# Optimization experiments

Measured on AMD Instinct MI355X. Metric: run time of the kernel, lower is better.

The kernel has to match this reference:

```python
import jax, jax.numpy as jnp
import numpy as np

NH = 16

def sinusoidal_pos(pos, nh=NH):
    # pos: [B, L] -> P: [B, L, nh], interleaved sin/cos with integer multiples of pi
    freqs = jnp.arange(1, nh // 2 + 1, dtype=pos.dtype) * jnp.pi  # [nh/2]
    ang = pos[..., None] * freqs                                   # [B, L, nh/2]
    # interleave: even channels sin, odd channels cos
    P = jnp.stack([jnp.sin(ang), jnp.cos(ang)], axis=-1)           # [B, L, nh/2, 2]
    return P.reshape(*pos.shape, nh)


def setup_inputs() -> dict:
    key = jax.random.key(0)
    k1, k2, k3, k4, k5, k6 = jax.random.split(key, 6)
    B, L, nx, nh = 2048, 1024, 8, NH
    return {
        "x": jax.random.normal(k1, (B, L, nx), dtype=jnp.float32),
        "pos": jax.random.uniform(k2, (B, L), dtype=jnp.float32),
        "W_q": jax.random.normal(k3, (nh, nx), dtype=jnp.float32) * 0.1,
        "W_k": jax.random.normal(k4, (nh, nx), dtype=jnp.float32) * 0.1,
        "W_v": jax.random.normal(k5, (nh, nx), dtype=jnp.float32) * 0.1,
        "W_o": jax.random.normal(k6, (nh, nh), dtype=jnp.float32) * 0.1,
    }


def reference(x, pos, W_q, W_k, W_v, W_o):
    # x: [B, L, nx]; pos: [B, L]; Linear weights are [out, in] (torch convention)
    q = jnp.einsum("blx,hx->blh", x, W_q)
    k = jnp.einsum("blx,hx->blh", x, W_k)
    v = jnp.einsum("blx,hx->blh", x, W_v)
    P = sinusoidal_pos(pos, W_q.shape[0])
    q = q + P
    k = k + P
    L = q.shape[1]
    # channel-wise attention: score over feature dim, [B, nh, nh]
    score = jnp.einsum("bld,ble->bde", q, k) / jnp.sqrt(jnp.asarray(L, q.dtype))
    attn = jax.nn.softmax(score, axis=-1)
    out = jnp.einsum("bde,ble->bdl", attn, v)   # [B, nh, L]
    out = jnp.einsum("bdl,hd->blh", out, W_o)   # transpose then W_o: [B, L, nh]
    return out
```

## Files before the change

kernel.cpp:

```cpp
#include <hip/hip_runtime.h>
#include <cstdint>
#include <cstddef>

#define LSEQ 1024
#define NH   16
#define NX   8

__global__ __launch_bounds__(256, 1)
void attn_moments4(const float* __restrict__ x, const float* __restrict__ pos,
                   const float* __restrict__ Wq, const float* __restrict__ Wk,
                   const float* __restrict__ Wv, const float* __restrict__ Wo,
                   float* __restrict__ out) {
    __shared__ float sums[256];
    __shared__ float U_s[128];
    __shared__ float score_s[256];
    __shared__ float attn_s[256];
    __shared__ float M_s[256];
    __shared__ float weff_s[128];

    const int tid  = threadIdx.x;
    const int w    = tid >> 6;
    const int lane = tid & 63;
    const int b    = blockIdx.x;
    const float* xb = x   + (size_t)b * LSEQ * NX;
    const float* pb = pos + (size_t)b * LSEQ;

    float A[52];
    #pragma unroll
    for (int i = 0; i < 52; ++i) A[i] = 0.f;

    for (int i = 0; i < 16; ++i) {
        const int l = i * 64 + lane;
        const float4 a = *(const float4*)(xb + (size_t)l * 8);
        const float4 c = *(const float4*)(xb + (size_t)l * 8 + 4);
        const float pv = pb[l];
        const float px[8] = {a.x, a.y, a.z, a.w, c.x, c.y, c.z, c.w};
        const float s1 = sinpif(pv), c1 = cospif(pv);
        const float c2x = 2.f * c1;

        if (w == 0) {
            #pragma unroll
            for (int p = 0; p < 8; ++p)
                #pragma unroll
                for (int q = p; q < 8; ++q)
                    A[p * 8 - (p * (p - 1)) / 2 + (q - p)] += px[p] * px[q];
            float s = s1, cc = c1, sp = 0.f, cp = 1.f;
            #pragma unroll
            for (int m = 1; m <= 16; ++m) {
                if (m > 1) { const float sn = c2x*s - sp, cn = c2x*cc - cp;
                             sp = s; cp = cc; s = sn; cc = cn; }
                A[35 + m] += s;
            }
        } else if (w == 1) {
            float s = s1, cc = c1, sp = 0.f, cp = 1.f;
            #pragma unroll
            for (int m = 1; m <= 16; ++m) {
                if (m > 1) { const float sn = c2x*s - sp, cn = c2x*cc - cp;
                             sp = s; cp = cc; s = sn; cc = cn; }
                A[m - 1] += cc;
                if (m <= 8) {
                    A[16 + 2*(m-1)] += px[0] * s;  A[16 + 2*m - 1] += px[0] * cc;
                    A[32 + 2*(m-1)] += px[1] * s;  A[32 + 2*m - 1] += px[1] * cc;
                }
            }
        } else if (w == 2) {
            float s = s1, cc = c1, sp = 0.f, cp = 1.f;
            #pragma unroll
            for (int m = 1; m <= 8; ++m) {
                if (m > 1) { const float sn = c2x*s - sp, cn = c2x*cc - cp;
                             sp = s; cp = cc; s = sn; cc = cn; }
                A[ 0 + 2*(m-1)] += px[2] * s;  A[ 0 + 2*m - 1] += px[2] * cc;
                A[16 + 2*(m-1)] += px[3] * s;  A[16 + 2*m - 1] += px[3] * cc;
                A[32 + 2*(m-1)] += px[4] * s;  A[32 + 2*m - 1] += px[4] * cc;
            }
        } else {
            float s = s1, cc = c1, sp = 0.f, cp = 1.f;
            #pragma unroll
            for (int m = 1; m <= 8; ++m) {
                if (m > 1) { const float sn = c2x*s - sp, cn = c2x*cc - cp;
                             sp = s; cp = cc; s = sn; cc = cn; }
                A[ 0 + 2*(m-1)] += px[5] * s;  A[ 0 + 2*m - 1] += px[5] * cc;
                A[16 + 2*(m-1)] += px[6] * s;  A[16 + 2*m - 1] += px[6] * cc;
                A[32 + 2*(m-1)] += px[7] * s;  A[32 + 2*m - 1] += px[7] * cc;
            }
        }
    }

    if (w == 0) {
        #pragma unroll
        for (int j = 0; j < 52; ++j) {
            float v = A[j];
            v += __shfl_xor(v, 1);  v += __shfl_xor(v, 2);  v += __shfl_xor(v, 4);
            v += __shfl_xor(v, 8);  v += __shfl_xor(v, 16); v += __shfl_xor(v, 32);
            if (lane == 0) sums[j < 36 ? j : 128 + j] = v;
        }
    } else if (w == 1) {
        #pragma unroll
        for (int j = 0; j < 48; ++j) {
            float v = A[j];
            v += __shfl_xor(v, 1);  v += __shfl_xor(v, 2);  v += __shfl_xor(v, 4);
            v += __shfl_xor(v, 8);  v += __shfl_xor(v, 16); v += __shfl_xor(v, 32);
            if (lane == 0) sums[j < 16 ? 180 + j : 20 + j] = v;
        }
    } else if (w == 2) {
        #pragma unroll
        for (int j = 0; j < 48; ++j) {
            float v = A[j];
            v += __shfl_xor(v, 1);  v += __shfl_xor(v, 2);  v += __shfl_xor(v, 4);
            v += __shfl_xor(v, 8);  v += __shfl_xor(v, 16); v += __shfl_xor(v, 32);
            if (lane == 0) sums[68 + j] = v;
        }
    } else {
        #pragma unroll
        for (int j = 0; j < 48; ++j) {
            float v = A[j];
            v += __shfl_xor(v, 1);  v += __shfl_xor(v, 2);  v += __shfl_xor(v, 4);
            v += __shfl_xor(v, 8);  v += __shfl_xor(v, 16); v += __shfl_xor(v, 32);
            if (lane == 0) sums[116 + j] = v;
        }
    }
    __syncthreads();

    if (tid < 128) {
        const int d = tid >> 3, y = tid & 7;
        float acc = 0.f;
        #pragma unroll
        for (int xx = 0; xx < 8; ++xx) {
            const int p = xx < y ? xx : y;
            const int q = xx < y ? y : xx;
            acc += Wq[d * 8 + xx] * sums[8 * p - (p * (p - 1)) / 2 + (q - p)];
        }
        U_s[tid] = acc;
    }
    __syncthreads();
    {
        const int d = tid >> 4, e = tid & 15;
        float a1 = 0.f, a2 = 0.f, a3 = 0.f;
        #pragma unroll
        for (int y = 0; y < 8; ++y) a1 += U_s[d * 8 + y] * Wk[e * 8 + y];
        #pragma unroll
        for (int xx = 0; xx < 8; ++xx) {
            a2 += Wq[d * 8 + xx] * sums[36 + xx * 16 + e];
            a3 += Wk[e * 8 + xx] * sums[36 + xx * 16 + d];
        }
        const int fi = (d >> 1) + 1, fj = (e >> 1) + 1;
        const int spd = fi + fj;
        const int smd = fi > fj ? fi - fj : fj - fi;
        const float Smp = sums[163 + spd];
        const float Cmp = sums[179 + spd];
        const float Sms = (smd == 0) ? 0.f : sums[163 + smd];
        const float Cms = (smd == 0) ? (float)LSEQ : sums[179 + smd];
        const bool de = !(d & 1), ee = !(e & 1);
        float Dv;
        if (de && ee)       Dv = 0.5f * (Cms - Cmp);
        else if (de && !ee) Dv = 0.5f * (Smp + (fi >= fj ? 1.f : -1.f) * Sms);
        else if (!de && ee) Dv = 0.5f * (Smp + (fj >= fi ? 1.f : -1.f) * Sms);
        else                Dv = 0.5f * (Cms + Cmp);
        score_s[tid] = (a1 + a2 + a3 + Dv) * 0.03125f;
    }
    __syncthreads();

    if (tid < 16) {
        float mx = -1e30f;
        #pragma unroll
        for (int e = 0; e < 16; ++e) mx = fmaxf(mx, score_s[tid * 16 + e]);
        float ex[16], sum = 0.f;
        #pragma unroll
        for (int e = 0; e < 16; ++e) { ex[e] = __expf(score_s[tid * 16 + e] - mx); sum += ex[e]; }
        const float inv = 1.f / sum;
        #pragma unroll
        for (int e = 0; e < 16; ++e) attn_s[tid * 16 + e] = ex[e] * inv;
    }
    __syncthreads();
    {
        const int h = tid >> 4, e = tid & 15;
        float acc = 0.f;
        #pragma unroll
        for (int d = 0; d < 16; ++d) acc += Wo[h * 16 + d] * attn_s[d * 16 + e];
        M_s[tid] = acc;
    }
    __syncthreads();
    if (tid < 128) {
        const int h = tid >> 3, xx = tid & 7;
        float acc = 0.f;
        #pragma unroll
        for (int e = 0; e < 16; ++e) acc += M_s[h * 16 + e] * Wv[e * 8 + xx];
        weff_s[tid] = acc;
    }
    __syncthreads();

    #pragma unroll
    for (int pass = 0; pass < 2; ++pass) {
        float xr[2][8];
        #pragma unroll
        for (int r = 0; r < 2; ++r) {
            const int l = pass * 512 + r * 256 + tid;
            const float4 a = *(const float4*)(xb + (size_t)l * 8);
            const float4 c = *(const float4*)(xb + (size_t)l * 8 + 4);
            xr[r][0]=a.x; xr[r][1]=a.y; xr[r][2]=a.z; xr[r][3]=a.w;
            xr[r][4]=c.x; xr[r][5]=c.y; xr[r][6]=c.z; xr[r][7]=c.w;
        }
        float o[2][16];
        #pragma unroll
        for (int h = 0; h < 16; ++h) {
            const float4 wA = *(const float4*)(weff_s + h * 8);
            const float4 wB = *(const float4*)(weff_s + h * 8 + 4);
            #pragma unroll
            for (int r = 0; r < 2; ++r) {
                o[r][h] = xr[r][0]*wA.x + xr[r][1]*wA.y + xr[r][2]*wA.z + xr[r][3]*wA.w
                        + xr[r][4]*wB.x + xr[r][5]*wB.y + xr[r][6]*wB.z + xr[r][7]*wB.w;
            }
        }
        #pragma unroll
        for (int r = 0; r < 2; ++r) {
            const int l = pass * 512 + r * 256 + tid;
            const size_t base = ((size_t)b * LSEQ + l) * NH;
            #pragma unroll
            for (int g = 0; g < 4; ++g)
                *(float4*)(out + base + g * 4) =
                    make_float4(o[r][g*4+0], o[r][g*4+1], o[r][g*4+2], o[r][g*4+3]);
        }
    }
}

extern "C" void kernel_launch(void* const* d_in, const int* in_sizes, int n_in,
                              void* d_out, int out_size, void* d_ws, size_t ws_size,
                              hipStream_t stream) {
    const float* x   = (const float*)d_in[0];
    const float* pos = (const float*)d_in[1];
    const float* Wq  = (const float*)d_in[2];
    const float* Wk  = (const float*)d_in[3];
    const float* Wv  = (const float*)d_in[4];
    const float* Wo  = (const float*)d_in[5];
    float* out = (float*)d_out;
    const int B = in_sizes[1] / LSEQ;
    attn_moments4<<<B, 256, 0, stream>>>(x, pos, Wq, Wk, Wv, Wo, out);
}
```

Baseline: 101.5 us.

## Split per-batch moments into two chunks across two kernels with workspace reduction

Each batch's moment accumulation is split across two blocks, each handling half the sequence. The partial sums go to a global workspace, and a second kernel adds the halves, computes the attention matrix, and writes half the output per block. The aim is more parallelism (4096 blocks instead of 2048) and a shorter serial accumulation loop per block. In exchange it adds a second launch, workspace traffic, redundant small attention setup in each finish block, and a second read of x. The original fused kernel is kept as a fallback when the workspace is too small.

```diff
diff --git a/kernel.cpp b/kernel.cpp
--- a/kernel.cpp
+++ b/kernel.cpp
@@ -2,15 +2,132 @@
 #include <cstdint>
 #include <cstddef>
 
-#define LSEQ 1024
-#define NH   16
-#define NX   8
+#define LSEQ   1024
+#define NH     16
+#define NX     8
+#define CHUNKS 2
+#define RPB    512
+
 
 __global__ __launch_bounds__(256, 1)
-void attn_moments4(const float* __restrict__ x, const float* __restrict__ pos,
+void moments_kernel(const float* __restrict__ x, const float* __restrict__ pos,
+                    float* __restrict__ g_part) {
+    __shared__ float sums[256];
+    const int tid  = threadIdx.x;
+    const int w    = tid >> 6;
+    const int lane = tid & 63;
+    const int bid  = blockIdx.x;
+    const int b    = bid >> 1;
+    const int c    = bid & 1;
+    const float* xb = x   + ((size_t)b * LSEQ + c * RPB) * NX;
+    const float* pb = pos + (size_t)b * LSEQ + c * RPB;
+
+    sums[tid] = 0.f;
+
+    float A[52];
+    #pragma unroll
+    for (int i = 0; i < 52; ++i) A[i] = 0.f;
+
+    for (int i = 0; i < RPB / 64; ++i) {
+        const int l = i * 64 + lane;
+        const float4 a = *(const float4*)(xb + (size_t)l * 8);
+        const float4 cv = *(const float4*)(xb + (size_t)l * 8 + 4);
+        const float pv = pb[l];
+        const float px[8] = {a.x, a.y, a.z, a.w, cv.x, cv.y, cv.z, cv.w};
+        const float s1 = sinpif(pv), c1 = cospif(pv);
+        const float c2x = 2.f * c1;
+
+        if (w == 0) {
+            #pragma unroll
+            for (int p = 0; p < 8; ++p)
+                #pragma unroll
+                for (int q = p; q < 8; ++q)
+                    A[p * 8 - (p * (p - 1)) / 2 + (q - p)] += px[p] * px[q];
+            float s = s1, cc = c1, sp = 0.f, cp = 1.f;
+            #pragma unroll
+            for (int m = 1; m <= 16; ++m) {
+                if (m > 1) { const float sn = c2x*s - sp, cn = c2x*cc - cp;
+                             sp = s; cp = cc; s = sn; cc = cn; }
+                A[35 + m] += s;
+            }
+        } else if (w == 1) {
+            float s = s1, cc = c1, sp = 0.f, cp = 1.f;
+            #pragma unroll
+            for (int m = 1; m <= 16; ++m) {
+                if (m > 1) { const float sn = c2x*s - sp, cn = c2x*cc - cp;
+                             sp = s; cp = cc; s = sn; cc = cn; }
+                A[m - 1] += cc;
+                if (m <= 8) {
+                    A[16 + 2*(m-1)] += px[0] * s;  A[16 + 2*m - 1] += px[0] * cc;
+                    A[32 + 2*(m-1)] += px[1] * s;  A[32 + 2*m - 1] += px[1] * cc;
+                }
+            }
+        } else if (w == 2) {
+            float s = s1, cc = c1, sp = 0.f, cp = 1.f;
+            #pragma unroll
+            for (int m = 1; m <= 8; ++m) {
+                if (m > 1) { const float sn = c2x*s - sp, cn = c2x*cc - cp;
+                             sp = s; cp = cc; s = sn; cc = cn; }
+                A[ 0 + 2*(m-1)] += px[2] * s;  A[ 0 + 2*m - 1] += px[2] * cc;
+                A[16 + 2*(m-1)] += px[3] * s;  A[16 + 2*m - 1] += px[3] * cc;
+                A[32 + 2*(m-1)] += px[4] * s;  A[32 + 2*m - 1] += px[4] * cc;
+            }
+        } else {
+            float s = s1, cc = c1, sp = 0.f, cp = 1.f;
+            #pragma unroll
+            for (int m = 1; m <= 8; ++m) {
+                if (m > 1) { const float sn = c2x*s - sp, cn = c2x*cc - cp;
+                             sp = s; cp = cc; s = sn; cc = cn; }
+                A[ 0 + 2*(m-1)] += px[5] * s;  A[ 0 + 2*m - 1] += px[5] * cc;
+                A[16 + 2*(m-1)] += px[6] * s;  A[16 + 2*m - 1] += px[6] * cc;
+                A[32 + 2*(m-1)] += px[7] * s;  A[32 + 2*m - 1] += px[7] * cc;
+            }
+        }
+    }
+
+    __syncthreads();
+    if (w == 0) {
+        #pragma unroll
+        for (int j = 0; j < 52; ++j) {
+            float v = A[j];
+            v += __shfl_xor(v, 1);  v += __shfl_xor(v, 2);  v += __shfl_xor(v, 4);
+            v += __shfl_xor(v, 8);  v += __shfl_xor(v, 16); v += __shfl_xor(v, 32);
+            if (lane == 0) sums[j < 36 ? j : 128 + j] = v;
+        }
+    } else if (w == 1) {
+        #pragma unroll
+        for (int j = 0; j < 48; ++j) {
+            float v = A[j];
+            v += __shfl_xor(v, 1);  v += __shfl_xor(v, 2);  v += __shfl_xor(v, 4);
+            v += __shfl_xor(v, 8);  v += __shfl_xor(v, 16); v += __shfl_xor(v, 32);
+            if (lane == 0) sums[j < 16 ? 180 + j : 20 + j] = v;
+        }
+    } else if (w == 2) {
+        #pragma unroll
+        for (int j = 0; j < 48; ++j) {
+            float v = A[j];
+            v += __shfl_xor(v, 1);  v += __shfl_xor(v, 2);  v += __shfl_xor(v, 4);
+            v += __shfl_xor(v, 8);  v += __shfl_xor(v, 16); v += __shfl_xor(v, 32);
+            if (lane == 0) sums[68 + j] = v;
+        }
+    } else {
+        #pragma unroll
+        for (int j = 0; j < 48; ++j) {
+            float v = A[j];
+            v += __shfl_xor(v, 1);  v += __shfl_xor(v, 2);  v += __shfl_xor(v, 4);
+            v += __shfl_xor(v, 8);  v += __shfl_xor(v, 16); v += __shfl_xor(v, 32);
+            if (lane == 0) sums[116 + j] = v;
+        }
+    }
+    __syncthreads();
+    g_part[(size_t)bid * 256 + tid] = sums[tid];
+}
+
+__global__ __launch_bounds__(256, 1)
+void finish_kernel(const float* __restrict__ x,
                    const float* __restrict__ Wq, const float* __restrict__ Wk,
                    const float* __restrict__ Wv, const float* __restrict__ Wo,
-                   float* __restrict__ out) {
+                   const float* __restrict__ g_part, float* __restrict__ out) {
     __shared__ float sums[256];
     __shared__ float U_s[128];
     __shared__ float score_s[256];
@@ -18,107 +135,14 @@
     __shared__ float M_s[256];
     __shared__ float weff_s[128];
 
-    const int tid  = threadIdx.x;
-    const int w    = tid >> 6;
-    const int lane = tid & 63;
-    const int b    = blockIdx.x;
-    const float* xb = x   + (size_t)b * LSEQ * NX;
-    const float* pb = pos + (size_t)b * LSEQ;
-
-    float A[52];
-    #pragma unroll
-    for (int i = 0; i < 52; ++i) A[i] = 0.f;
-
-    for (int i = 0; i < 16; ++i) {
-        const int l = i * 64 + lane;
-        const float4 a = *(const float4*)(xb + (size_t)l * 8);
-        const float4 c = *(const float4*)(xb + (size_t)l * 8 + 4);
-        const float pv = pb[l];
-        const float px[8] = {a.x, a.y, a.z, a.w, c.x, c.y, c.z, c.w};
-        const float s1 = sinpif(pv), c1 = cospif(pv);
-        const float c2x = 2.f * c1;
-
-        if (w == 0) {
-            #pragma unroll
-            for (int p = 0; p < 8; ++p)
-                #pragma unroll
-                for (int q = p; q < 8; ++q)
-                    A[p * 8 - (p * (p - 1)) / 2 + (q - p)] += px[p] * px[q];
-            float s = s1, cc = c1, sp = 0.f, cp = 1.f;
-            #pragma unroll
-            for (int m = 1; m <= 16; ++m) {
-                if (m > 1) { const float sn = c2x*s - sp, cn = c2x*cc - cp;
-                             sp = s; cp = cc; s = sn; cc = cn; }
-                A[35 + m] += s;
-            }
-        } else if (w == 1) {
-            float s = s1, cc = c1, sp = 0.f, cp = 1.f;
-            #pragma unroll
-            for (int m = 1; m <= 16; ++m) {
-                if (m > 1) { const float sn = c2x*s - sp, cn = c2x*cc - cp;
-                             sp = s; cp = cc; s = sn; cc = cn; }
-                A[m - 1] += cc;
-                if (m <= 8) {
-                    A[16 + 2*(m-1)] += px[0] * s;  A[16 + 2*m - 1] += px[0] * cc;
-                    A[32 + 2*(m-1)] += px[1] * s;  A[32 + 2*m - 1] += px[1] * cc;
-                }
-            }
-        } else if (w == 2) {
-            float s = s1, cc = c1, sp = 0.f, cp = 1.f;
-            #pragma unroll
-            for (int m = 1; m <= 8; ++m) {
-                if (m > 1) { const float sn = c2x*s - sp, cn = c2x*cc - cp;
-                             sp = s; cp = cc; s = sn; cc = cn; }
-                A[ 0 + 2*(m-1)] += px[2] * s;  A[ 0 + 2*m - 1] += px[2] * cc;
-                A[16 + 2*(m-1)] += px[3] * s;  A[16 + 2*m - 1] += px[3] * cc;
-                A[32 + 2*(m-1)] += px[4] * s;  A[32 + 2*m - 1] += px[4] * cc;
-            }
-        } else {
-            float s = s1, cc = c1, sp = 0.f, cp = 1.f;
-            #pragma unroll
-            for (int m = 1; m <= 8; ++m) {
-                if (m > 1) { const float sn = c2x*s - sp, cn = c2x*cc - cp;
-                             sp = s; cp = cc; s = sn; cc = cn; }
-                A[ 0 + 2*(m-1)] += px[5] * s;  A[ 0 + 2*m - 1] += px[5] * cc;
-                A[16 + 2*(m-1)] += px[6] * s;  A[16 + 2*m - 1] += px[6] * cc;
-                A[32 + 2*(m-1)] += px[7] * s;  A[32 + 2*m - 1] += px[7] * cc;
-            }
-        }
-    }
-
-    if (w == 0) {
-        #pragma unroll
-        for (int j = 0; j < 52; ++j) {
-            float v = A[j];
-            v += __shfl_xor(v, 1);  v += __shfl_xor(v, 2);  v += __shfl_xor(v, 4);
-            v += __shfl_xor(v, 8);  v += __shfl_xor(v, 16); v += __shfl_xor(v, 32);
-            if (lane == 0) sums[j < 36 ? j : 128 + j] = v;
-        }
-    } else if (w == 1) {
-        #pragma unroll
-        for (int j = 0; j < 48; ++j) {
-            float v = A[j];
-            v += __shfl_xor(v, 1);  v += __shfl_xor(v, 2);  v += __shfl_xor(v, 4);
-            v += __shfl_xor(v, 8);  v += __shfl_xor(v, 16); v += __shfl_xor(v, 32);
-            if (lane == 0) sums[j < 16 ? 180 + j : 20 + j] = v;
-        }
-    } else if (w == 2) {
-        #pragma unroll
-        for (int j = 0; j < 48; ++j) {
-            float v = A[j];
-            v += __shfl_xor(v, 1);  v += __shfl_xor(v, 2);  v += __shfl_xor(v, 4);
-            v += __shfl_xor(v, 8);  v += __shfl_xor(v, 16); v += __shfl_xor(v, 32);
-            if (lane == 0) sums[68 + j] = v;
-        }
-    } else {
-        #pragma unroll
-        for (int j = 0; j < 48; ++j) {
-            float v = A[j];
-            v += __shfl_xor(v, 1);  v += __shfl_xor(v, 2);  v += __shfl_xor(v, 4);
-            v += __shfl_xor(v, 8);  v += __shfl_xor(v, 16); v += __shfl_xor(v, 32);
-            if (lane == 0) sums[116 + j] = v;
-        }
-    }
+    const int tid = threadIdx.x;
+    const int bid = blockIdx.x;
+    const int b   = bid >> 1;
+    const int c   = bid & 1;
+    const float* xb = x + (size_t)b * LSEQ * NX;
+
+    sums[tid] = g_part[(size_t)(b * 2) * 256 + tid]
+              + g_part[(size_t)(b * 2 + 1) * 256 + tid];
     __syncthreads();
 
     if (tid < 128) {
@@ -189,6 +213,217 @@
     }
     __syncthreads();
 
+    {
+        float xr[2][8];
+        #pragma unroll
+        for (int r = 0; r < 2; ++r) {
+            const int l = c * RPB + r * 256 + tid;
+            const float4 a = *(const float4*)(xb + (size_t)l * 8);
+            const float4 cv = *(const float4*)(xb + (size_t)l * 8 + 4);
+            xr[r][0]=a.x; xr[r][1]=a.y; xr[r][2]=a.z; xr[r][3]=a.w;
+            xr[r][4]=cv.x; xr[r][5]=cv.y; xr[r][6]=cv.z; xr[r][7]=cv.w;
+        }
+        float o[2][16];
+        #pragma unroll
+        for (int h = 0; h < 16; ++h) {
+            const float4 wA = *(const float4*)(weff_s + h * 8);
+            const float4 wB = *(const float4*)(weff_s + h * 8 + 4);
+            #pragma unroll
+            for (int r = 0; r < 2; ++r) {
+                o[r][h] = xr[r][0]*wA.x + xr[r][1]*wA.y + xr[r][2]*wA.z + xr[r][3]*wA.w
+                        + xr[r][4]*wB.x + xr[r][5]*wB.y + xr[r][6]*wB.z + xr[r][7]*wB.w;
+            }
+        }
+        #pragma unroll
+        for (int r = 0; r < 2; ++r) {
+            const int l = c * RPB + r * 256 + tid;
+            const size_t base = ((size_t)b * LSEQ + l) * NH;
+            #pragma unroll
+            for (int g = 0; g < 4; ++g)
+                *(float4*)(out + base + g * 4) =
+                    make_float4(o[r][g*4+0], o[r][g*4+1], o[r][g*4+2], o[r][g*4+3]);
+        }
+    }
+}
+
+__global__ __launch_bounds__(256, 1)
+void attn_moments4(const float* __restrict__ x, const float* __restrict__ pos,
+                   const float* __restrict__ Wq, const float* __restrict__ Wk,
+                   const float* __restrict__ Wv, const float* __restrict__ Wo,
+                   float* __restrict__ out) {
+    __shared__ float sums[256];
+    __shared__ float U_s[128];
+    __shared__ float score_s[256];
+    __shared__ float attn_s[256];
+    __shared__ float M_s[256];
+    __shared__ float weff_s[128];
+
+    const int tid  = threadIdx.x;
+    const int w    = tid >> 6;
+    const int lane = tid & 63;
+    const int b    = blockIdx.x;
+    const float* xb = x   + (size_t)b * LSEQ * NX;
+    const float* pb = pos + (size_t)b * LSEQ;
+
+    float A[52];
+    #pragma unroll
+    for (int i = 0; i < 52; ++i) A[i] = 0.f;
+
+    for (int i = 0; i < 16; ++i) {
+        const int l = i * 64 + lane;
+        const float4 a = *(const float4*)(xb + (size_t)l * 8);
+        const float4 cv = *(const float4*)(xb + (size_t)l * 8 + 4);
+        const float pv = pb[l];
+        const float px[8] = {a.x, a.y, a.z, a.w, cv.x, cv.y, cv.z, cv.w};
+        const float s1 = sinpif(pv), c1 = cospif(pv);
+        const float c2x = 2.f * c1;
+        if (w == 0) {
+            #pragma unroll
+            for (int p = 0; p < 8; ++p)
+                #pragma unroll
+                for (int q = p; q < 8; ++q)
+                    A[p * 8 - (p * (p - 1)) / 2 + (q - p)] += px[p] * px[q];
+            float s = s1, cc = c1, sp = 0.f, cp = 1.f;
+            #pragma unroll
+            for (int m = 1; m <= 16; ++m) {
+                if (m > 1) { const float sn = c2x*s - sp, cn = c2x*cc - cp;
+                             sp = s; cp = cc; s = sn; cc = cn; }
+                A[35 + m] += s;
+            }
+        } else if (w == 1) {
+            float s = s1, cc = c1, sp = 0.f, cp = 1.f;
+            #pragma unroll
+            for (int m = 1; m <= 16; ++m) {
+                if (m > 1) { const float sn = c2x*s - sp, cn = c2x*cc - cp;
+                             sp = s; cp = cc; s = sn; cc = cn; }
+                A[m - 1] += cc;
+                if (m <= 8) {
+                    A[16 + 2*(m-1)] += px[0] * s;  A[16 + 2*m - 1] += px[0] * cc;
+                    A[32 + 2*(m-1)] += px[1] * s;  A[32 + 2*m - 1] += px[1] * cc;
+                }
+            }
+        } else if (w == 2) {
+            float s = s1, cc = c1, sp = 0.f, cp = 1.f;
+            #pragma unroll
+            for (int m = 1; m <= 8; ++m) {
+                if (m > 1) { const float sn = c2x*s - sp, cn = c2x*cc - cp;
+                             sp = s; cp = cc; s = sn; cc = cn; }
+                A[ 0 + 2*(m-1)] += px[2] * s;  A[ 0 + 2*m - 1] += px[2] * cc;
+                A[16 + 2*(m-1)] += px[3] * s;  A[16 + 2*m - 1] += px[3] * cc;
+                A[32 + 2*(m-1)] += px[4] * s;  A[32 + 2*m - 1] += px[4] * cc;
+            }
+        } else {
+            float s = s1, cc = c1, sp = 0.f, cp = 1.f;
+            #pragma unroll
+            for (int m = 1; m <= 8; ++m) {
+                if (m > 1) { const float sn = c2x*s - sp, cn = c2x*cc - cp;
+                             sp = s; cp = cc; s = sn; cc = cn; }
+                A[ 0 + 2*(m-1)] += px[5] * s;  A[ 0 + 2*m - 1] += px[5] * cc;
+                A[16 + 2*(m-1)] += px[6] * s;  A[16 + 2*m - 1] += px[6] * cc;
+                A[32 + 2*(m-1)] += px[7] * s;  A[32 + 2*m - 1] += px[7] * cc;
+            }
+        }
+    }
+    if (w == 0) {
+        #pragma unroll
+        for (int j = 0; j < 52; ++j) {
+            float v = A[j];
+            v += __shfl_xor(v, 1);  v += __shfl_xor(v, 2);  v += __shfl_xor(v, 4);
+            v += __shfl_xor(v, 8);  v += __shfl_xor(v, 16); v += __shfl_xor(v, 32);
+            if (lane == 0) sums[j < 36 ? j : 128 + j] = v;
+        }
+    } else if (w == 1) {
+        #pragma unroll
+        for (int j = 0; j < 48; ++j) {
+            float v = A[j];
+            v += __shfl_xor(v, 1);  v += __shfl_xor(v, 2);  v += __shfl_xor(v, 4);
+            v += __shfl_xor(v, 8);  v += __shfl_xor(v, 16); v += __shfl_xor(v, 32);
+            if (lane == 0) sums[j < 16 ? 180 + j : 20 + j] = v;
+        }
+    } else if (w == 2) {
+        #pragma unroll
+        for (int j = 0; j < 48; ++j) {
+            float v = A[j];
+            v += __shfl_xor(v, 1);  v += __shfl_xor(v, 2);  v += __shfl_xor(v, 4);
+            v += __shfl_xor(v, 8);  v += __shfl_xor(v, 16); v += __shfl_xor(v, 32);
+            if (lane == 0) sums[68 + j] = v;
+        }
+    } else {
+        #pragma unroll
+        for (int j = 0; j < 48; ++j) {
+            float v = A[j];
+            v += __shfl_xor(v, 1);  v += __shfl_xor(v, 2);  v += __shfl_xor(v, 4);
+            v += __shfl_xor(v, 8);  v += __shfl_xor(v, 16); v += __shfl_xor(v, 32);
+            if (lane == 0) sums[116 + j] = v;
+        }
+    }
+    __syncthreads();
+    if (tid < 128) {
+        const int d = tid >> 3, y = tid & 7;
+        float acc = 0.f;
+        #pragma unroll
+        for (int xx = 0; xx < 8; ++xx) {
+            const int p = xx < y ? xx : y;
+            const int q = xx < y ? y : xx;
+            acc += Wq[d * 8 + xx] * sums[8 * p - (p * (p - 1)) / 2 + (q - p)];
+        }
+        U_s[tid] = acc;
+    }
+    __syncthreads();
+    {
+        const int d = tid >> 4, e = tid & 15;
+        float a1 = 0.f, a2 = 0.f, a3 = 0.f;
+        #pragma unroll
+        for (int y = 0; y < 8; ++y) a1 += U_s[d * 8 + y] * Wk[e * 8 + y];
+        #pragma unroll
+        for (int xx = 0; xx < 8; ++xx) {
+            a2 += Wq[d * 8 + xx] * sums[36 + xx * 16 + e];
+            a3 += Wk[e * 8 + xx] * sums[36 + xx * 16 + d];
+        }
+        const int fi = (d >> 1) + 1, fj = (e >> 1) + 1;
+        const int spd = fi + fj;
+        const int smd = fi > fj ? fi - fj : fj - fi;
+        const float Smp = sums[163 + spd];
+        const float Cmp = sums[179 + spd];
+        const float Sms = (smd == 0) ? 0.f : sums[163 + smd];
+        const float Cms = (smd == 0) ? (float)LSEQ : sums[179 + smd];
+        const bool de = !(d & 1), ee = !(e & 1);
+        float Dv;
+        if (de && ee)       Dv = 0.5f * (Cms - Cmp);
+        else if (de && !ee) Dv = 0.5f * (Smp + (fi >= fj ? 1.f : -1.f) * Sms);
+        else if (!de && ee) Dv = 0.5f * (Smp + (fj >= fi ? 1.f : -1.f) * Sms);
+        else                Dv = 0.5f * (Cms + Cmp);
+        score_s[tid] = (a1 + a2 + a3 + Dv) * 0.03125f;
+    }
+    __syncthreads();
+    if (tid < 16) {
+        float mx = -1e30f;
+        #pragma unroll
+        for (int e = 0; e < 16; ++e) mx = fmaxf(mx, score_s[tid * 16 + e]);
+        float ex[16], sum = 0.f;
+        #pragma unroll
+        for (int e = 0; e < 16; ++e) { ex[e] = __expf(score_s[tid * 16 + e] - mx); sum += ex[e]; }
+        const float inv = 1.f / sum;
+        #pragma unroll
+        for (int e = 0; e < 16; ++e) attn_s[tid * 16 + e] = ex[e] * inv;
+    }
+    __syncthreads();
+    {
+        const int h = tid >> 4, e = tid & 15;
+        float acc = 0.f;
+        #pragma unroll
+        for (int d = 0; d < 16; ++d) acc += Wo[h * 16 + d] * attn_s[d * 16 + e];
+        M_s[tid] = acc;
+    }
+    __syncthreads();
+    if (tid < 128) {
+        const int h = tid >> 3, xx = tid & 7;
+        float acc = 0.f;
+        #pragma unroll
+        for (int e = 0; e < 16; ++e) acc += M_s[h * 16 + e] * Wv[e * 8 + xx];
+        weff_s[tid] = acc;
+    }
+    __syncthreads();
     #pragma unroll
     for (int pass = 0; pass < 2; ++pass) {
         float xr[2][8];
@@ -196,9 +431,9 @@
         for (int r = 0; r < 2; ++r) {
             const int l = pass * 512 + r * 256 + tid;
             const float4 a = *(const float4*)(xb + (size_t)l * 8);
-            const float4 c = *(const float4*)(xb + (size_t)l * 8 + 4);
+            const float4 cv = *(const float4*)(xb + (size_t)l * 8 + 4);
             xr[r][0]=a.x; xr[r][1]=a.y; xr[r][2]=a.z; xr[r][3]=a.w;
-            xr[r][4]=c.x; xr[r][5]=c.y; xr[r][6]=c.z; xr[r][7]=c.w;
+            xr[r][4]=cv.x; xr[r][5]=cv.y; xr[r][6]=cv.z; xr[r][7]=cv.w;
         }
         float o[2][16];
         #pragma unroll
@@ -234,5 +469,13 @@
     const float* Wo  = (const float*)d_in[5];
     float* out = (float*)d_out;
     const int B = in_sizes[1] / LSEQ;
-    attn_moments4<<<B, 256, 0, stream>>>(x, pos, Wq, Wk, Wv, Wo, out);
+
+    const size_t ws_needed = (size_t)B * CHUNKS * 256 * sizeof(float);
+    if (ws_size >= ws_needed) {
+        float* g_part = (float*)d_ws;
+        moments_kernel<<<B * CHUNKS, 256, 0, stream>>>(x, pos, g_part);
+        finish_kernel<<<B * CHUNKS, 256, 0, stream>>>(x, Wq, Wk, Wv, Wo, g_part, out);
+    } else {
+        attn_moments4<<<B, 256, 0, stream>>>(x, pos, Wq, Wk, Wv, Wo, out);
+    }
 }
```

Result: slower. 128.7 us (+26.8%).
